# Kernel optimization log

Hardware: AMD Instinct MI355X
Metric: run time of the kernel (lower is better)

Reference implementation:

```python
import jax, jax.numpy as jnp
import numpy as np

D_MODEL = 1024
NUM_HEADS = 16
D_K = D_MODEL // NUM_HEADS
SCALE = 1.0 / np.sqrt(D_K).astype(np.float32)


def _rope_cos_sin(T, d_k):
    inv_freq = 1.0 / (10000.0 ** (jnp.arange(0, d_k, 2, dtype=jnp.float32) / d_k))
    t = jnp.arange(T, dtype=jnp.float32)
    freqs = jnp.outer(t, inv_freq)                      # [T, d_k/2]
    emb = jnp.concatenate([freqs, freqs], axis=-1)      # [T, d_k]
    return jnp.cos(emb)[None, None], jnp.sin(emb)[None, None]  # [1,1,T,d_k]


def _rotate_half(x):
    x1, x2 = x[..., : x.shape[-1] // 2], x[..., x.shape[-1] // 2 :]
    return jnp.concatenate([-x2, x1], axis=-1)


def setup_inputs() -> dict:
    key = jax.random.key(0)
    ks = jax.random.split(key, 8)
    B, T, C = 2, 2048, D_MODEL
    x = jax.random.normal(ks[0], (B, T, C), dtype=jnp.float32)
    # torch nn.Linear weights are [out, in]; forward does x @ W.T
    s = 1.0 / np.sqrt(C)
    Wq = jax.random.uniform(ks[1], (C, C), jnp.float32, -s, s)
    Wk = jax.random.uniform(ks[2], (C, C), jnp.float32, -s, s)
    Wv = jax.random.uniform(ks[3], (C, C), jnp.float32, -s, s)
    Wo = jax.random.uniform(ks[4], (C, C), jnp.float32, -s, s)
    bo = jax.random.uniform(ks[5], (C,), jnp.float32, -s, s)
    sector_bias = jnp.zeros((1, NUM_HEADS, 1, 1), dtype=jnp.float32)
    sector_weights = jax.random.uniform(ks[6], (B, T), jnp.float32, 0.5, 1.5)
    # causal mask, broadcastable to [B,H,T,T]; 0 -> masked
    mask = jnp.tril(jnp.ones((T, T), dtype=jnp.int32))[None, None]
    return {
        "x": x, "Wq": Wq, "Wk": Wk, "Wv": Wv, "Wo": Wo, "bo": bo,
        "sector_bias": sector_bias, "sector_weights": sector_weights,
        "mask": mask,
    }


def reference(x, Wq, Wk, Wv, Wo, bo, sector_bias, sector_weights, mask):
    B, T, C = x.shape
    H, dk = NUM_HEADS, D_K
    q = (x @ Wq.T).reshape(B, T, H, dk).transpose(0, 2, 1, 3)  # [B,H,T,dk]
    k = (x @ Wk.T).reshape(B, T, H, dk).transpose(0, 2, 1, 3)
    v = (x @ Wv.T).reshape(B, T, H, dk).transpose(0, 2, 1, 3)
    cos, sin = _rope_cos_sin(T, dk)
    q = q * cos + _rotate_half(q) * sin
    k = k * cos + _rotate_half(k) * sin
    scores = jnp.einsum("bhqd,bhkd->bhqk", q, k) * SCALE
    scores = scores + sector_bias
    scores = scores * sector_weights[:, None, None, :]  # broadcast over key dim
    scores = jnp.where(mask == 0, -jnp.inf, scores)
    attn = jax.nn.softmax(scores, axis=-1)
    out = jnp.einsum("bhqk,bhkd->bhqd", attn, v)
    out = out.transpose(0, 2, 1, 3).reshape(B, T, C)
    return out @ Wo.T + bo
```

## Files before the change

### kernel.cpp

```cpp
#include <hip/hip_runtime.h>


typedef __bf16 bf16x8 __attribute__((ext_vector_type(8)));
typedef float f32x4 __attribute__((ext_vector_type(4)));
typedef float f32x16 __attribute__((ext_vector_type(16)));
typedef unsigned short u16x8 __attribute__((ext_vector_type(8)));

__device__ __forceinline__ unsigned short f2bf(float f) {
    union { float f; unsigned int u; } c; c.f = f;
    unsigned int u = c.u;
    unsigned int r = u + 0x7fffu + ((u >> 16) & 1u);
    return (unsigned short)(r >> 16);
}
__device__ __forceinline__ unsigned cvtpk(float lo, float hi) {
    unsigned r;
    asm("v_cvt_pk_bf16_f32 %0, %1, %2" : "=v"(r) : "v"(lo), "v"(hi));
    return r;
}
__device__ __forceinline__ void plswap(unsigned a, unsigned b, unsigned& r0, unsigned& r1) {
#if __has_builtin(__builtin_amdgcn_permlane32_swap)
    auto s = __builtin_amdgcn_permlane32_swap(a, b, false, false);
    r0 = (unsigned)s[0]; r1 = (unsigned)s[1];
#else
    const int hh = (int)(threadIdx.x & 63) >> 5;
    const unsigned oa = (unsigned)__shfl_xor((int)a, 32);
    const unsigned ob = (unsigned)__shfl_xor((int)b, 32);
    r0 = hh ? ob : a;
    r1 = hh ? b : oa;
#endif
}
__device__ __forceinline__ void stage8_f32(unsigned short* dst, const float* src) {
    const float4 a = *(const float4*)src;
    const float4 b = *(const float4*)(src + 4);
    u16x8 v;
    v[0] = f2bf(a.x); v[1] = f2bf(a.y); v[2] = f2bf(a.z); v[3] = f2bf(a.w);
    v[4] = f2bf(b.x); v[5] = f2bf(b.y); v[6] = f2bf(b.z); v[7] = f2bf(b.w);
    *(u16x8*)dst = v;
}
__device__ __forceinline__ void async16(const unsigned short* g, unsigned short* l) {
    __builtin_amdgcn_global_load_lds(
        (const __attribute__((address_space(1))) void*)g,
        (__attribute__((address_space(3))) void*)l, 16, 0, 0);
}

__global__ __launch_bounds__(256) void cvt_all(
    const float* __restrict__ x, const float* __restrict__ Wq, const float* __restrict__ Wk,
    const float* __restrict__ Wv, const float* __restrict__ Wo,
    unsigned short* __restrict__ dst, int hasX, int n8)
{
    const int i = blockIdx.x * 256 + threadIdx.x;
    if (i >= n8) return;
    int r = i;
    const float* src; int off;
    const int xg = hasX ? 524288 : 0;
    if (r < xg) { src = x; off = r; }
    else {
        r -= xg;
        const int w = r >> 17, o = r & 131071;
        src = (w == 0) ? Wq : (w == 1) ? Wk : (w == 2) ? Wv : Wo;
        off = o;
    }
    stage8_f32(&dst[(size_t)i * 8], &src[(size_t)off * 8]);
}

template<int A_BF16>
__global__ __launch_bounds__(256) void gemm_qkv(
    const void* __restrict__ Av, const unsigned short* __restrict__ Wb,
    unsigned short* __restrict__ outv, const float* __restrict__ swg)
{
    constexpr int K = 1024, BK = 32;
    __shared__ __align__(16) unsigned short As[3][128 * BK];
    __shared__ __align__(16) unsigned short Bs[3][128 * BK];
    const int tid = threadIdx.x;
    const int wid = tid >> 6, lane = tid & 63, g = lane >> 4, l = lane & 15;
    const int wm = (wid & 1) * 64, wn = (wid >> 1) * 64;

    const int lin = blockIdx.x + (blockIdx.y << 3) + (blockIdx.z << 8);
    const int wg  = (lin & 7) * 96 + (lin >> 3);
    const int bx = wg & 7, by = (wg >> 3) & 31, bz = wg >> 8;
    const int m0 = by * 128, n0 = bx * 128;
    const int z = bz;
    const unsigned short* W = Wb + (size_t)z * 1048576;

    f32x4 acc[4][4];
#pragma unroll
    for (int i = 0; i < 4; ++i)
#pragma unroll
        for (int j = 0; j < 4; ++j) acc[i][j] = f32x4{0.f, 0.f, 0.f, 0.f};

    const int r  = tid >> 2;
    const int cs = (((tid & 3) ^ ((tid >> 3) & 3)) * 8);
    const int xg = (g ^ ((l >> 1) & 3)) * 8;
    int aoff[4], boff[4];
#pragma unroll
    for (int im = 0; im < 4; ++im) aoff[im] = (wm + im * 16 + l) * BK + xg;
#pragma unroll
    for (int in = 0; in < 4; ++in) boff[in] = (wn + in * 16 + l) * BK + xg;

    const unsigned short* Wg0 = &W[(size_t)(n0 + r) * K + cs];
    const unsigned short* Wg1 = Wg0 + (size_t)64 * K;

    auto compute = [&](int buf) {
        bf16x8 af[4], bfr[4];
#pragma unroll
        for (int im = 0; im < 4; ++im) af[im]  = *(const bf16x8*)&As[buf][aoff[im]];
#pragma unroll
        for (int in = 0; in < 4; ++in) bfr[in] = *(const bf16x8*)&Bs[buf][boff[in]];
#pragma unroll
        for (int im = 0; im < 4; ++im)
#pragma unroll
            for (int in = 0; in < 4; ++in)
                acc[im][in] = __builtin_amdgcn_mfma_f32_16x16x32_bf16(af[im], bfr[in], acc[im][in], 0, 0, 0);
    };

    if (A_BF16) {
        const unsigned short* A = (const unsigned short*)Av;
        const unsigned short* Ag0 = &A[(size_t)(m0 + r) * K + cs];
        const unsigned short* Ag1 = Ag0 + (size_t)64 * K;
        auto stage = [&](int buf, int k0) {
            unsigned short* AsW = &As[buf][wid * 512];
            async16(Ag0 + k0, AsW);
            async16(Ag1 + k0, AsW + 2048);
            unsigned short* BsW = &Bs[buf][wid * 512];
            async16(Wg0 + k0, BsW);
            async16(Wg1 + k0, BsW + 2048);
        };
        stage(0, 0);
        stage(1, BK);
        for (int t = 0; t < 10; ++t) {
            const int tb = t * 96;
#pragma unroll
            for (int u = 0; u < 3; ++u) {
                asm volatile("s_waitcnt vmcnt(4)" ::: "memory");
                __builtin_amdgcn_s_barrier();
                compute(u);
                stage((u + 2) % 3, tb + (u + 2) * BK);
            }
        }
        asm volatile("s_waitcnt vmcnt(4)" ::: "memory");
        __builtin_amdgcn_s_barrier();
        compute(0);
        asm volatile("s_waitcnt vmcnt(0)" ::: "memory");
        __builtin_amdgcn_s_barrier();
        compute(1);
    } else {
        auto stageF = [&](int buf, int k0) {
            const float* A = (const float*)Av;
            stage8_f32(&As[buf][(tid >> 2) * BK + cs],        &A[(size_t)(m0 + r) * K + k0 + cs]);
            stage8_f32(&As[buf][(tid >> 2) * BK + cs + 2048], &A[(size_t)(m0 + 64 + r) * K + k0 + cs]);
            unsigned short* BsW = &Bs[buf][wid * 512];
            async16(Wg0 + k0, BsW);
            async16(Wg1 + k0, BsW + 2048);
        };
        stageF(0, 0);
        __syncthreads();
        for (int k0 = 0; k0 < K; k0 += BK) {
            const int cur = (k0 >> 5) & 1;
            if (k0 + BK < K) stageF(cur ^ 1, k0 + BK);
            compute(cur);
            __syncthreads();
        }
    }

    unsigned short* outq = outv + (size_t)z * 4194304;
    if (z < 2) {
        const int hq = (n0 + wn) >> 6;
        float freq[2];
#pragma unroll
        for (int in = 0; in < 2; ++in)
            freq[in] = exp2f(-(float)(in * 16 + l) * 0.41524101186f);
#pragma unroll
        for (int im = 0; im < 4; ++im)
#pragma unroll
            for (int i = 0; i < 4; ++i) {
                const int m = m0 + wm + im * 16 + g * 4 + i;
                const int b = m >> 11, t = m & 2047;
                float fw = 1.0f;
                if (z == 1) fw = 0.18033688011f * swg[(b << 11) + t];
                const size_t fq = (size_t)((b << 4) + hq) * 131072
                                + (size_t)((t >> 5) << 2) * 512
                                + (size_t)((((l >> 3) & 1) << 5) + (t & 31)) * 8 + (l & 7);
#pragma unroll
                for (int in = 0; in < 2; ++in) {
                    const float ang = (float)t * freq[in];
                    const float cs2 = __cosf(ang), sn = __sinf(ang);
                    const float x1 = acc[im][in][i], x2 = acc[im][in + 2][i];
                    outq[fq + (size_t)in * 512]       = f2bf((x1 * cs2 - x2 * sn) * fw);
                    outq[fq + (size_t)(in + 2) * 512] = f2bf((x2 * cs2 + x1 * sn) * fw);
                }
            }
    } else {
#pragma unroll
        for (int im = 0; im < 4; ++im)
#pragma unroll
            for (int in = 0; in < 4; ++in) {
                const int n = n0 + wn + in * 16 + l;
                const int h = n >> 6, d = n & 63;
                const int mb = m0 + wm + im * 16 + g * 4;
                const int bq = mb >> 11, t0 = mb & 2047;
                ushort4 pk;
                pk.x = f2bf(acc[im][in][0]); pk.y = f2bf(acc[im][in][1]);
                pk.z = f2bf(acc[im][in][2]); pk.w = f2bf(acc[im][in][3]);
                const size_t fv = (size_t)((bq << 4) + h) * 131072
                                + (size_t)(((t0 >> 5) << 2) + ((d >> 5) << 1) + ((t0 >> 4) & 1)) * 512
                                + (size_t)((((t0 >> 3) & 1) << 5) + (d & 31)) * 8 + (t0 & 7);
                *(ushort4*)&outq[fv] = pk;
            }
    }
}

__global__ __launch_bounds__(256) void gemm_proj(
    const unsigned short* __restrict__ A, const unsigned short* __restrict__ W,
    float* __restrict__ out, const float* __restrict__ bias)
{
    constexpr int K = 1024, BK = 32;
    __shared__ __align__(16) unsigned short As[3][64 * BK];
    __shared__ __align__(16) unsigned short Bs[3][128 * BK];
    const int tid = threadIdx.x;
    const int wid = tid >> 6, lane = tid & 63, g = lane >> 4, l = lane & 15;
    const int wm = (wid & 1) * 32, wn = (wid >> 1) * 64;

    const int lin = blockIdx.x + (blockIdx.y << 3);
    const int wg  = (lin & 7) * 64 + (lin >> 3);
    const int m0 = (wg >> 3) * 64, n0 = (wg & 7) * 128;

    f32x4 acc[2][4];
#pragma unroll
    for (int i = 0; i < 2; ++i)
#pragma unroll
        for (int j = 0; j < 4; ++j) acc[i][j] = f32x4{0.f, 0.f, 0.f, 0.f};

    const int r  = tid >> 2;
    const int cs = (((tid & 3) ^ ((tid >> 3) & 3)) * 8);
    const int xg = (g ^ ((l >> 1) & 3)) * 8;
    int aoff[2], boff[4];
#pragma unroll
    for (int im = 0; im < 2; ++im) aoff[im] = (wm + im * 16 + l) * BK + xg;
#pragma unroll
    for (int in = 0; in < 4; ++in) boff[in] = (wn + in * 16 + l) * BK + xg;

    const unsigned short* Ag0 = &A[(size_t)(m0 + r) * K + cs];
    const unsigned short* Wg0 = &W[(size_t)(n0 + r) * K + cs];
    const unsigned short* Wg1 = Wg0 + (size_t)64 * K;

    auto stage = [&](int buf, int k0) {
        async16(Ag0 + k0, &As[buf][wid * 512]);
        unsigned short* BsW = &Bs[buf][wid * 512];
        async16(Wg0 + k0, BsW);
        async16(Wg1 + k0, BsW + 2048);
    };
    auto compute = [&](int buf) {
        bf16x8 af[2], bfr[4];
#pragma unroll
        for (int im = 0; im < 2; ++im) af[im]  = *(const bf16x8*)&As[buf][aoff[im]];
#pragma unroll
        for (int in = 0; in < 4; ++in) bfr[in] = *(const bf16x8*)&Bs[buf][boff[in]];
#pragma unroll
        for (int im = 0; im < 2; ++im)
#pragma unroll
            for (int in = 0; in < 4; ++in)
                acc[im][in] = __builtin_amdgcn_mfma_f32_16x16x32_bf16(af[im], bfr[in], acc[im][in], 0, 0, 0);
    };

    stage(0, 0);
    stage(1, BK);
    for (int t = 0; t < 10; ++t) {
        const int tb = t * 96;
#pragma unroll
        for (int u = 0; u < 3; ++u) {
            asm volatile("s_waitcnt vmcnt(3)" ::: "memory");
            __builtin_amdgcn_s_barrier();
            compute(u);
            stage((u + 2) % 3, tb + (u + 2) * BK);
        }
    }
    asm volatile("s_waitcnt vmcnt(3)" ::: "memory");
    __builtin_amdgcn_s_barrier();
    compute(0);
    asm volatile("s_waitcnt vmcnt(0)" ::: "memory");
    __builtin_amdgcn_s_barrier();
    compute(1);

#pragma unroll
    for (int im = 0; im < 2; ++im)
#pragma unroll
        for (int in = 0; in < 4; ++in) {
            const int n = n0 + wn + in * 16 + l;
#pragma unroll
            for (int i = 0; i < 4; ++i) {
                const int m = m0 + wm + im * 16 + g * 4 + i;
                out[(size_t)m * 1024 + n] = acc[im][in][i] + bias[n];
            }
        }
}

__global__ __launch_bounds__(128, 2) void flash_attn(
    const unsigned short* __restrict__ Qf, const unsigned short* __restrict__ Kf,
    const unsigned short* __restrict__ Vf, const float* __restrict__ sbias,
    const float* __restrict__ sw, unsigned short* __restrict__ attn)
{
    constexpr int T = 2048;
    __shared__ float Cmb[3072];

    const int tid = threadIdx.x, wid = tid >> 6, lane = tid & 63;
    const int hl = lane & 31, hh = lane >> 5;
    const int id = blockIdx.x;
    const int p  = 63 - (id >> 5);
    const int bh = id & 31, b = bh >> 4, h = bh & 15;
    const size_t fb = (size_t)bh * 131072;
    const float bias = sbias[h];
    const float* swb = sw + b * T;

    bf16x8 onef;
#pragma unroll
    for (int j = 0; j < 8; ++j) onef[j] = (__bf16)1.0f;

    const int q0 = p * 32;
    bf16x8 qf[4];
#pragma unroll
    for (int ks = 0; ks < 4; ++ks)
        qf[ks] = *(const bf16x8*)&Qf[fb + (size_t)(p * 4 + ks) * 512 + lane * 8];

    f32x16 oacc[2], lrow;
#pragma unroll
    for (int r = 0; r < 16; ++r) { oacc[0][r] = 0.f; oacc[1][r] = 0.f; lrow[r] = 0.f; }

    for (int c = wid; c <= p; c += 2) {
        const unsigned short* kb = &Kf[fb + (size_t)c * 2048 + lane * 8];
        const unsigned short* vb = &Vf[fb + (size_t)c * 2048 + lane * 8];

        const bf16x8 kf0 = *(const bf16x8*)&kb[0];
        const bf16x8 kf1 = *(const bf16x8*)&kb[512];
        const bf16x8 kf2 = *(const bf16x8*)&kb[1024];
        const bf16x8 kf3 = *(const bf16x8*)&kb[1536];
        f32x16 sx;
#pragma unroll
        for (int r = 0; r < 16; ++r) sx[r] = 0.f;
        sx = __builtin_amdgcn_mfma_f32_32x32x16_bf16(kf0, qf[0], sx, 0, 0, 0);
        sx = __builtin_amdgcn_mfma_f32_32x32x16_bf16(kf1, qf[1], sx, 0, 0, 0);
        sx = __builtin_amdgcn_mfma_f32_32x32x16_bf16(kf2, qf[2], sx, 0, 0, 0);
        sx = __builtin_amdgcn_mfma_f32_32x32x16_bf16(kf3, qf[3], sx, 0, 0, 0);

        const bf16x8 vf00 = *(const bf16x8*)&vb[0];
        const bf16x8 vf01 = *(const bf16x8*)&vb[512];
        const bf16x8 vf10 = *(const bf16x8*)&vb[1024];
        const bf16x8 vf11 = *(const bf16x8*)&vb[1536];

        if (bias != 0.0f) {
            const float bn = bias * 1.44269504f;
#pragma unroll
            for (int r = 0; r < 16; ++r) {
                const int kl = (r & 3) + 8 * (r >> 2) + 4 * hh;
                sx[r] += bn * swb[c * 32 + kl];
            }
        }
        if (c == p) {
#pragma unroll
            for (int r = 0; r < 16; ++r) {
                const int kl = (r & 3) + 8 * (r >> 2) + 4 * hh;
                sx[r] = (kl <= hl) ? sx[r] : -1e30f;
            }
        }
#pragma unroll
        for (int r = 0; r < 16; ++r) sx[r] = exp2f(sx[r]);

        unsigned wds[8];
#pragma unroll
        for (int g2 = 0; g2 < 4; ++g2) {
            wds[g2 * 2]     = cvtpk(sx[g2 * 4],     sx[g2 * 4 + 1]);
            wds[g2 * 2 + 1] = cvtpk(sx[g2 * 4 + 2], sx[g2 * 4 + 3]);
        }
        bf16x8 pf[2];
#pragma unroll
        for (int ks = 0; ks < 2; ++ks) {
            unsigned a0, a1, b0, b1;
            plswap(wds[4 * ks],     wds[4 * ks + 2], a0, a1);
            plswap(wds[4 * ks + 1], wds[4 * ks + 3], b0, b1);
            union { unsigned u[4]; bf16x8 v; } pk_;
            pk_.u[0] = a0; pk_.u[1] = b0;
            pk_.u[2] = a1; pk_.u[3] = b1;
            pf[ks] = pk_.v;
        }

        lrow = __builtin_amdgcn_mfma_f32_32x32x16_bf16(pf[0], onef, lrow, 0, 0, 0);
        lrow = __builtin_amdgcn_mfma_f32_32x32x16_bf16(pf[1], onef, lrow, 0, 0, 0);

        oacc[0] = __builtin_amdgcn_mfma_f32_32x32x16_bf16(pf[0], vf00, oacc[0], 0, 0, 0);
        oacc[0] = __builtin_amdgcn_mfma_f32_32x32x16_bf16(pf[1], vf01, oacc[0], 0, 0, 0);
        oacc[1] = __builtin_amdgcn_mfma_f32_32x32x16_bf16(pf[0], vf10, oacc[1], 0, 0, 0);
        oacc[1] = __builtin_amdgcn_mfma_f32_32x32x16_bf16(pf[1], vf11, oacc[1], 0, 0, 0);
    }

    __syncthreads();
    if (wid == 1) {
#pragma unroll
        for (int dt = 0; dt < 2; ++dt)
#pragma unroll
            for (int r = 0; r < 16; ++r) Cmb[(dt * 16 + r) * 64 + lane] = oacc[dt][r];
#pragma unroll
        for (int r = 0; r < 16; ++r) Cmb[2048 + r * 64 + lane] = lrow[r];
    }
    __syncthreads();
    if (wid == 0) {
#pragma unroll
        for (int r = 0; r < 16; ++r) {
            const float li = 1.0f / (lrow[r] + Cmb[2048 + r * 64 + lane]);
            const int row = (r & 3) + 8 * (r >> 2) + 4 * hh;
            const int qr = q0 + row;
#pragma unroll
            for (int dt = 0; dt < 2; ++dt) {
                const float ov = oacc[dt][r] + Cmb[(dt * 16 + r) * 64 + lane];
                attn[(size_t)(b * T + qr) * 1024 + h * 64 + dt * 32 + hl] = f2bf(ov * li);
            }
        }
    }
}

extern "C" void kernel_launch(void* const* d_in, const int* in_sizes, int n_in,
                              void* d_out, int out_size, void* d_ws, size_t ws_size,
                              hipStream_t stream) {
    const float* x  = (const float*)d_in[0];
    const float* Wq = (const float*)d_in[1];
    const float* Wk = (const float*)d_in[2];
    const float* Wv = (const float*)d_in[3];
    const float* Wo = (const float*)d_in[4];
    const float* bo = (const float*)d_in[5];
    const float* sb = (const float*)d_in[6];
    const float* sw = (const float*)d_in[7];

    const size_t QKV_SZ = 4194304;
    const size_t W_SZ   = 1048576;
    unsigned short* ws16 = (unsigned short*)d_ws;
    const bool big = ws_size >= 2 * (4 * QKV_SZ + 4 * W_SZ);

    if (big) {
        unsigned short* xb    = ws16;
        unsigned short* Wb3   = xb + QKV_SZ;
        unsigned short* Wob   = Wb3 + 3 * W_SZ;
        unsigned short* qkv   = Wob + W_SZ;
        unsigned short* attnb = xb;

        cvt_all<<<4096, 256, 0, stream>>>(x, Wq, Wk, Wv, Wo, xb, 1, 1048576);
        gemm_qkv<1><<<dim3(8, 32, 3), 256, 0, stream>>>(xb, Wb3, qkv, sw);
        flash_attn<<<2048, 128, 0, stream>>>(qkv, qkv + QKV_SZ, qkv + 2 * QKV_SZ,
                                             sb, sw, attnb);
        gemm_proj<<<dim3(8, 64), 256, 0, stream>>>(attnb, Wob, (float*)d_out, bo);
    } else {
        unsigned short* qkv   = ws16;
        unsigned short* attnb = qkv + 3 * QKV_SZ;
        unsigned short* Wb3   = attnb;
        unsigned short* Wob   = qkv;

        cvt_all<<<1536, 256, 0, stream>>>(x, Wq, Wk, Wv, Wo, Wb3, 0, 393216);
        gemm_qkv<0><<<dim3(8, 32, 3), 256, 0, stream>>>(x, Wb3, qkv, sw);
        flash_attn<<<2048, 128, 0, stream>>>(qkv, qkv + QKV_SZ, qkv + 2 * QKV_SZ,
                                             sb, sw, attnb);
        cvt_all<<<512, 256, 0, stream>>>(x, Wo, Wo, Wo, Wo, Wob, 0, 131072);
        gemm_proj<<<dim3(8, 64), 256, 0, stream>>>(attnb, Wob, (float*)d_out, bo);
    }
}
```

Baseline: 191.3 us.

## Pre-swizzle x and QKV weights into MFMA fragment layout and skip LDS

The conversion kernel now writes x and Wq/Wk/Wv in a blocked layout that matches the MFMA 16x16x32 fragment order. The bf16 QKV GEMM then loads each operand fragment straight from global memory into registers, with no LDS staging, barriers or async-load pipeline. This removes LDS traffic and synchronisation. In exchange, operand tiles are no longer shared through LDS, so each wave fetches its own copies through the cache, and there is no explicit prefetch to hide global latency.

```diff
diff --git a/kernel.cpp b/kernel.cpp
--- a/kernel.cpp
+++ b/kernel.cpp
@@ -51,16 +51,23 @@
     const int i = blockIdx.x * 256 + threadIdx.x;
     if (i >= n8) return;
     int r = i;
-    const float* src; int off;
+    const float* src; size_t soff;
     const int xg = hasX ? 524288 : 0;
-    if (r < xg) { src = x; off = r; }
-    else {
+    if (r < xg) {
+        const int lane16 = r & 15, sub = (r >> 4) & 3, kb = (r >> 6) & 31, rb = r >> 11;
+        src = x; soff = (size_t)(rb * 16 + lane16) * 128 + kb * 4 + sub;
+    } else {
         r -= xg;
         const int w = r >> 17, o = r & 131071;
         src = (w == 0) ? Wq : (w == 1) ? Wk : (w == 2) ? Wv : Wo;
-        off = o;
-    }
-    stage8_f32(&dst[(size_t)i * 8], &src[(size_t)off * 8]);
+        if (hasX && w < 3) {
+            const int lane16 = o & 15, sub = (o >> 4) & 3, kb = (o >> 6) & 31, nb = o >> 11;
+            soff = (size_t)(nb * 16 + lane16) * 128 + kb * 4 + sub;
+        } else {
+            soff = o;
+        }
+    }
+    stage8_f32(&dst[(size_t)i * 8], &src[soff * 8]);
 }
 
 template<int A_BF16>
@@ -69,8 +76,6 @@
     unsigned short* __restrict__ outv, const float* __restrict__ swg)
 {
     constexpr int K = 1024, BK = 32;
-    __shared__ __align__(16) unsigned short As[3][128 * BK];
-    __shared__ __align__(16) unsigned short Bs[3][128 * BK];
     const int tid = threadIdx.x;
     const int wid = tid >> 6, lane = tid & 63, g = lane >> 4, l = lane & 15;
     const int wm = (wid & 1) * 64, wn = (wid >> 1) * 64;
@@ -88,62 +93,33 @@
 #pragma unroll
         for (int j = 0; j < 4; ++j) acc[i][j] = f32x4{0.f, 0.f, 0.f, 0.f};
 
-    const int r  = tid >> 2;
-    const int cs = (((tid & 3) ^ ((tid >> 3) & 3)) * 8);
-    const int xg = (g ^ ((l >> 1) & 3)) * 8;
-    int aoff[4], boff[4];
-#pragma unroll
-    for (int im = 0; im < 4; ++im) aoff[im] = (wm + im * 16 + l) * BK + xg;
-#pragma unroll
-    for (int in = 0; in < 4; ++in) boff[in] = (wn + in * 16 + l) * BK + xg;
-
-    const unsigned short* Wg0 = &W[(size_t)(n0 + r) * K + cs];
-    const unsigned short* Wg1 = Wg0 + (size_t)64 * K;
-
-    auto compute = [&](int buf) {
-        bf16x8 af[4], bfr[4];
-#pragma unroll
-        for (int im = 0; im < 4; ++im) af[im]  = *(const bf16x8*)&As[buf][aoff[im]];
-#pragma unroll
-        for (int in = 0; in < 4; ++in) bfr[in] = *(const bf16x8*)&Bs[buf][boff[in]];
-#pragma unroll
-        for (int im = 0; im < 4; ++im)
+    if constexpr (A_BF16) {
+        const unsigned short* A = (const unsigned short*)Av;
+        const unsigned short* Ab = A + (size_t)((m0 + wm) >> 4) * 16384 + g * 128 + l * 8;
+        const unsigned short* Bb = W + (size_t)((n0 + wn) >> 4) * 16384 + g * 128 + l * 8;
+#pragma unroll 2
+        for (int kb = 0; kb < 32; ++kb) {
+            bf16x8 af[4], bfr[4];
+#pragma unroll
+            for (int im = 0; im < 4; ++im)
+                af[im]  = *(const bf16x8*)(Ab + (size_t)im * 16384 + kb * 512);
 #pragma unroll
             for (int in = 0; in < 4; ++in)
-                acc[im][in] = __builtin_amdgcn_mfma_f32_16x16x32_bf16(af[im], bfr[in], acc[im][in], 0, 0, 0);
-    };
-
-    if (A_BF16) {
-        const unsigned short* A = (const unsigned short*)Av;
-        const unsigned short* Ag0 = &A[(size_t)(m0 + r) * K + cs];
-        const unsigned short* Ag1 = Ag0 + (size_t)64 * K;
-        auto stage = [&](int buf, int k0) {
-            unsigned short* AsW = &As[buf][wid * 512];
-            async16(Ag0 + k0, AsW);
-            async16(Ag1 + k0, AsW + 2048);
-            unsigned short* BsW = &Bs[buf][wid * 512];
-            async16(Wg0 + k0, BsW);
-            async16(Wg1 + k0, BsW + 2048);
-        };
-        stage(0, 0);
-        stage(1, BK);
-        for (int t = 0; t < 10; ++t) {
-            const int tb = t * 96;
-#pragma unroll
-            for (int u = 0; u < 3; ++u) {
-                asm volatile("s_waitcnt vmcnt(4)" ::: "memory");
-                __builtin_amdgcn_s_barrier();
-                compute(u);
-                stage((u + 2) % 3, tb + (u + 2) * BK);
-            }
-        }
-        asm volatile("s_waitcnt vmcnt(4)" ::: "memory");
-        __builtin_amdgcn_s_barrier();
-        compute(0);
-        asm volatile("s_waitcnt vmcnt(0)" ::: "memory");
-        __builtin_amdgcn_s_barrier();
-        compute(1);
+                bfr[in] = *(const bf16x8*)(Bb + (size_t)in * 16384 + kb * 512);
+#pragma unroll
+            for (int im = 0; im < 4; ++im)
+#pragma unroll
+                for (int in = 0; in < 4; ++in)
+                    acc[im][in] = __builtin_amdgcn_mfma_f32_16x16x32_bf16(af[im], bfr[in], acc[im][in], 0, 0, 0);
+        }
     } else {
+        __shared__ __align__(16) unsigned short As[2][128 * BK];
+        __shared__ __align__(16) unsigned short Bs[2][128 * BK];
+        const int r  = tid >> 2;
+        const int cs = (((tid & 3) ^ ((tid >> 3) & 3)) * 8);
+        const int xg = (g ^ ((l >> 1) & 3)) * 8;
+        const unsigned short* Wg0 = &W[(size_t)(n0 + r) * K + cs];
+        const unsigned short* Wg1 = Wg0 + (size_t)64 * K;
         auto stageF = [&](int buf, int k0) {
             const float* A = (const float*)Av;
             stage8_f32(&As[buf][(tid >> 2) * BK + cs],        &A[(size_t)(m0 + r) * K + k0 + cs]);
@@ -157,7 +133,16 @@
         for (int k0 = 0; k0 < K; k0 += BK) {
             const int cur = (k0 >> 5) & 1;
             if (k0 + BK < K) stageF(cur ^ 1, k0 + BK);
-            compute(cur);
+            bf16x8 af[4], bfr[4];
+#pragma unroll
+            for (int im = 0; im < 4; ++im) af[im]  = *(const bf16x8*)&As[cur][(wm + im * 16 + l) * BK + xg];
+#pragma unroll
+            for (int in = 0; in < 4; ++in) bfr[in] = *(const bf16x8*)&Bs[cur][(wn + in * 16 + l) * BK + xg];
+#pragma unroll
+            for (int im = 0; im < 4; ++im)
+#pragma unroll
+                for (int in = 0; in < 4; ++in)
+                    acc[im][in] = __builtin_amdgcn_mfma_f32_16x16x32_bf16(af[im], bfr[in], acc[im][in], 0, 0, 0);
             __syncthreads();
         }
     }
@@ -173,7 +158,7 @@
         for (int im = 0; im < 4; ++im)
 #pragma unroll
             for (int i = 0; i < 4; ++i) {
-                const int m = m0 + wm + im * 16 + g * 4 + i;
+                const int m = m0 + wm + im * 16 + (lane >> 4) * 4 + i;
                 const int b = m >> 11, t = m & 2047;
                 float fw = 1.0f;
                 if (z == 1) fw = 0.18033688011f * swg[(b << 11) + t];
@@ -196,7 +181,7 @@
             for (int in = 0; in < 4; ++in) {
                 const int n = n0 + wn + in * 16 + l;
                 const int h = n >> 6, d = n & 63;
-                const int mb = m0 + wm + im * 16 + g * 4;
+                const int mb = m0 + wm + im * 16 + (lane >> 4) * 4;
                 const int bq = mb >> 11, t0 = mb & 2047;
                 ushort4 pk;
                 pk.x = f2bf(acc[im][in][0]); pk.y = f2bf(acc[im][in][1]);
```

Result: slower. 199.8 us (+4.5%).
